# Kernel tuning notes

Hardware: AMD Instinct MI355X
Metric: run time of the kernel (lower is better)

The kernel has to match this reference:

```python
import jax, jax.numpy as jnp
import numpy as np


def setup_inputs() -> dict:
    key = jax.random.key(0)
    k1, k2 = jax.random.split(key)
    N, K, D = 400000, 50, 256
    locF = jax.random.normal(k1, (N, 1, D), dtype=jnp.float32)
    Ck = jax.random.normal(k2, (1, K, D), dtype=jnp.float32)
    return {"locF": locF, "Ck": Ck}


def reference(locF, Ck):
    # locF: [N, 1, D], Ck: [1, k, D]
    x = locF[:, 0, :]            # [N, D]
    c = Ck[0]                    # [k, D]
    k, D = c.shape
    # mean squared distance: ((x - c)**2).mean(-1) expanded to avoid [N,k,D] intermediate
    x2 = jnp.sum(x * x, axis=1, keepdims=True)        # [N, 1]
    c2 = jnp.sum(c * c, axis=1)                       # [k]
    d2 = (x2 - 2.0 * (x @ c.T) + c2) / D              # [N, k]
    index = jnp.argmin(d2, axis=1)                    # [N]
    # single-pass scatter-add of sums and counts keyed by argmin
    sums = jax.ops.segment_sum(x, index, num_segments=k)   # [k, D]
    counts = jnp.zeros((k,), dtype=jnp.int32).at[index].add(1)
    Ck1 = sums[None]            # [1, k, D]  (matches torch.cat along dim=1 of [1,1,D] chunks)
    nItems = counts[None]       # [1, k]
    return Ck1, nItems
```

## Files before the change

kernel.cpp:

```cpp
#include <hip/hip_runtime.h>


typedef _Float16 f16x8 __attribute__((ext_vector_type(8)));
typedef float    f32x4 __attribute__((ext_vector_type(4)));
typedef float    f32x16 __attribute__((ext_vector_type(16)));
typedef int      i32x4 __attribute__((ext_vector_type(4)));
typedef unsigned int u32x4 __attribute__((ext_vector_type(4)));

constexpr int K = 50, KP = 64, D = 256, KD = K * D;
constexpr int BLK = 1024, GRID = 512, CH = 32;
constexpr int SST = 68;

#define VMCNT0 asm volatile("s_waitcnt vmcnt(0)" ::: "memory")
#define LGKM0  asm volatile("s_waitcnt lgkmcnt(0)" ::: "memory")
#define SBAR   { __builtin_amdgcn_sched_barrier(0); __builtin_amdgcn_s_barrier(); __builtin_amdgcn_sched_barrier(0); }

__global__ __launch_bounds__(BLK)
void k_fused(const float* __restrict__ x, const float* __restrict__ cc,
             float* __restrict__ partial, float* __restrict__ out,
             int N, int useAtomic) {
    __shared__ _Float16       sC[K * D];
    __shared__ unsigned short sxh[2][CH * D];
    __shared__ float          sS0[32 * SST];
    __shared__ float          sS1[32 * SST];
    __shared__ float          sc2[KP];
    __shared__ int            sidx[2][CH];
    __shared__ int            scnt[K];

    const int tid = threadIdx.x;
    for (int i = tid; i < K * D; i += BLK) sC[i] = (_Float16)0.f;
    if (tid < K) scnt[tid] = 0;
    __syncthreads();
    for (int i = tid; i < KD; i += BLK) {
        int r = i >> 8, col = i & 255, ch = col >> 3, wd = col & 7;
        sC[r * D + (((ch ^ (r & 7)) << 3) | wd)] = (_Float16)cc[i];
    }
    if (tid < KP) {
        float s = 0.f;
        if (tid < K) for (int q = 0; q < D; ++q) { float v = cc[tid * D + q]; s += v * v; }
        sc2[tid] = s;
    }
    __syncthreads();

    const int lane = tid & 63, ci = lane & 15, g = lane >> 4, w = tid >> 6;
    const int kh   = (w >= 14) ? 1 : 0;
    const int wA   = w & 1;
    const int ra   = lane & 31;
    const int dl   = lane >> 5;
    const int rakey = (ra & 7) ^ (((ra >> 3) & 1) << 2);
    const int cl32 = wA * 32 + (lane & 31);
    const int clkey = (lane & 31) & 7;
    const _Float16* cbp = &sC[(cl32 < K ? cl32 : K - 1) * D];
    const int bcol = w * 16 + ci, bc3 = bcol >> 3, bce = bcol & 7;

    const int nCh = N / CH;
    const int cpb = nCh / gridDim.x, rem = nCh % gridDim.x;
    const int bid = blockIdx.x;
    const int lo  = bid * cpb + (bid < rem ? bid : rem);
    const int cnt = cpb + (bid < rem ? 1 : 0);

    const float INF = 3.4e38f;
    const float c2A = (cl32 < K) ? sc2[cl32] : INF;

    const int srow = 2 * w + (lane >> 5);
    const int scol = (lane & 31);
    const int skey = (srow & 7) ^ (((srow >> 3) & 1) << 2);
    f32x4 rA = {0,0,0,0}, rB = {0,0,0,0};
#define ISSUE(t_) { const float* b_ = x + (size_t)(t_) * (CH * D) + srow * D + 8 * scol; \
    rA = *(const f32x4*)(b_); rB = *(const f32x4*)(b_ + 4); }
#define WSLOT(s_) { \
    f16x8 h_ = {(_Float16)rA[0], (_Float16)rA[1], (_Float16)rA[2], (_Float16)rA[3], \
                (_Float16)rB[0], (_Float16)rB[1], (_Float16)rB[2], (_Float16)rB[3]}; \
    *(f16x8*)(&sxh[s_][srow * D + ((scol ^ skey) << 3)]) = h_; }

    f32x4 bacc0 = {0,0,0,0}, bacc1 = {0,0,0,0}, bacc2 = {0,0,0,0}, bacc3 = {0,0,0,0};

    if (cnt > 0) { ISSUE(lo) VMCNT0; WSLOT(0) if (cnt > 1) ISSUE(lo + 1) }
    LGKM0; SBAR;

    for (int i = 0; i <= cnt; ++i) {
        if (w >= 12 && i < cnt) {
            const unsigned short* xb = &sxh[i & 1][0];
            f32x16 acc = {0,0,0,0,0,0,0,0,0,0,0,0,0,0,0,0};
#define A_KS(s) { \
            const int c_ = (kh * 8 + (s)) * 2 + dl; \
            f16x8 a = *(const f16x8*)(&xb[ra * D + ((c_ ^ rakey) << 3)]); \
            f16x8 b = *(const f16x8*)(cbp + ((c_ ^ clkey) << 3)); \
            acc = __builtin_amdgcn_mfma_f32_32x32x16_f16(a, b, acc, 0, 0, 0); }
            A_KS(0) A_KS(1) A_KS(2) A_KS(3) A_KS(4) A_KS(5) A_KS(6) A_KS(7)
#undef A_KS
            if (kh == 0) {
#define DUMP(r) { const int row_ = ((r) & 3) + 8 * ((r) >> 2) + 4 * dl; \
                sS0[row_ * SST + cl32] = c2A - 2.f * acc[r]; }
                DUMP(0) DUMP(1) DUMP(2) DUMP(3) DUMP(4) DUMP(5) DUMP(6) DUMP(7)
                DUMP(8) DUMP(9) DUMP(10) DUMP(11) DUMP(12) DUMP(13) DUMP(14) DUMP(15)
#undef DUMP
            } else {
#define DUMP(r) { const int row_ = ((r) & 3) + 8 * ((r) >> 2) + 4 * dl; \
                sS1[row_ * SST + cl32] = -2.f * acc[r]; }
                DUMP(0) DUMP(1) DUMP(2) DUMP(3) DUMP(4) DUMP(5) DUMP(6) DUMP(7)
                DUMP(8) DUMP(9) DUMP(10) DUMP(11) DUMP(12) DUMP(13) DUMP(14) DUMP(15)
#undef DUMP
            }
        }

        if (i >= 1) {
            const unsigned short* xbh = &sxh[(i - 1) & 1][0];
            const int jb = (i - 1) & 1;
            i32x4 idA = *(const i32x4*)(&sidx[jb][8 * g]);
            i32x4 idB = *(const i32x4*)(&sidx[jb][8 * g + 4]);
            unsigned short v0, v1, v2, v3, v4, v5, v6, v7;
#define RDH(j) { const int p_ = 8 * g + (j); const int key_ = (j) ^ ((g & 1) << 2); \
            v##j = xbh[p_ * D + ((bc3 ^ key_) << 3) + bce]; }
            RDH(0) RDH(1) RDH(2) RDH(3) RDH(4) RDH(5) RDH(6) RDH(7)
#undef RDH
            unsigned int w0 = (unsigned int)v0 | ((unsigned int)v1 << 16);
            unsigned int w1 = (unsigned int)v2 | ((unsigned int)v3 << 16);
            unsigned int w2 = (unsigned int)v4 | ((unsigned int)v5 << 16);
            unsigned int w3 = (unsigned int)v6 | ((unsigned int)v7 << 16);
            u32x4 W = {w0, w1, w2, w3};
            f16x8 bfr = __builtin_bit_cast(f16x8, W);
#define BMT(M, ACC) { \
            const int cl_ = (M) * 16 + ci; \
            f16x8 a = {(_Float16)(idA[0] == cl_ ? 1.f : 0.f), (_Float16)(idA[1] == cl_ ? 1.f : 0.f), \
                       (_Float16)(idA[2] == cl_ ? 1.f : 0.f), (_Float16)(idA[3] == cl_ ? 1.f : 0.f), \
                       (_Float16)(idB[0] == cl_ ? 1.f : 0.f), (_Float16)(idB[1] == cl_ ? 1.f : 0.f), \
                       (_Float16)(idB[2] == cl_ ? 1.f : 0.f), (_Float16)(idB[3] == cl_ ? 1.f : 0.f)}; \
            ACC = __builtin_amdgcn_mfma_f32_16x16x32_f16(a, bfr, ACC, 0, 0, 0); }
            BMT(0, bacc0) BMT(1, bacc1) BMT(2, bacc2) BMT(3, bacc3)
#undef BMT
        }

        LGKM0; SBAR;

        if (i + 1 < cnt) {
            VMCNT0;
            WSLOT((i + 1) & 1)
            if (i + 2 < cnt) ISSUE(lo + i + 2)
        }

        if (w >= 8 && w < 12 && i < cnt) {
            const int p_ = (w - 8) * 8 + (lane >> 3);
            const int q  = lane & 7;
            const float* s0p = &sS0[p_ * SST + 8 * q];
            const float* s1p = &sS1[p_ * SST + 8 * q];
            f32x4 a0 = *(const f32x4*)(s0p), a1 = *(const f32x4*)(s0p + 4);
            f32x4 b0 = *(const f32x4*)(s1p), b1 = *(const f32x4*)(s1p + 4);
            f32x4 u = a0 + b0, v = a1 + b1;
            float bm = u[0]; int bb = 8 * q;
#define CMP(VV, E, OFF) { float s_ = VV[E]; int c_ = 8 * q + (OFF); \
            if (s_ < bm) { bm = s_; bb = c_; } }
            CMP(u,1,1) CMP(u,2,2) CMP(u,3,3)
            CMP(v,0,4) CMP(v,1,5) CMP(v,2,6) CMP(v,3,7)
#undef CMP
            { float pm = __shfl_xor(bm, 1, 64); int pb = __shfl_xor(bb, 1, 64);
              if (pm < bm || (pm == bm && pb < bb)) { bm = pm; bb = pb; } }
            { float pm = __shfl_xor(bm, 2, 64); int pb = __shfl_xor(bb, 2, 64);
              if (pm < bm || (pm == bm && pb < bb)) { bm = pm; bb = pb; } }
            { float pm = __shfl_xor(bm, 4, 64); int pb = __shfl_xor(bb, 4, 64);
              if (pm < bm || (pm == bm && pb < bb)) { bm = pm; bb = pb; } }
            if (q == 0) { sidx[i & 1][p_] = bb; atomicAdd(&scnt[bb], 1); }
        }
        LGKM0; SBAR;
    }

    if (useAtomic) {
#define WBK(M, ACC) { \
        { int cl_ = (M)*16 + 4*g + 0; if (cl_ < K) atomicAdd(&out[cl_ * D + bcol], ACC[0]); } \
        { int cl_ = (M)*16 + 4*g + 1; if (cl_ < K) atomicAdd(&out[cl_ * D + bcol], ACC[1]); } \
        { int cl_ = (M)*16 + 4*g + 2; if (cl_ < K) atomicAdd(&out[cl_ * D + bcol], ACC[2]); } \
        { int cl_ = (M)*16 + 4*g + 3; if (cl_ < K) atomicAdd(&out[cl_ * D + bcol], ACC[3]); } }
        WBK(0, bacc0) WBK(1, bacc1) WBK(2, bacc2) WBK(3, bacc3)
#undef WBK
    } else {
        float* pb = partial + (size_t)bid * KD;
#define WBK(M, ACC) { \
        { int cl_ = (M)*16 + 4*g + 0; if (cl_ < K) pb[cl_ * D + bcol] = ACC[0]; } \
        { int cl_ = (M)*16 + 4*g + 1; if (cl_ < K) pb[cl_ * D + bcol] = ACC[1]; } \
        { int cl_ = (M)*16 + 4*g + 2; if (cl_ < K) pb[cl_ * D + bcol] = ACC[2]; } \
        { int cl_ = (M)*16 + 4*g + 3; if (cl_ < K) pb[cl_ * D + bcol] = ACC[3]; } }
        WBK(0, bacc0) WBK(1, bacc1) WBK(2, bacc2) WBK(3, bacc3)
#undef WBK
    }
    __syncthreads();
    for (int k = tid; k < K; k += BLK) atomicAdd(&out[KD + k], (float)scnt[k]);
}

__global__ __launch_bounds__(256)
void k_reduce(const float* __restrict__ partial, float* __restrict__ out, int G) {
    const int j  = blockIdx.x * 256 + threadIdx.x;
    const int bs = G / 8;
    const int b0 = blockIdx.y * bs;
    float s = 0.f;
    for (int b = b0; b < b0 + bs; ++b) s += partial[(size_t)b * KD + j];
    atomicAdd(&out[j], s);
}

extern "C" void kernel_launch(void* const* d_in, const int* in_sizes, int n_in,
                              void* d_out, int out_size, void* d_ws, size_t ws_size,
                              hipStream_t stream) {
    const float* x = (const float*)d_in[0];
    const float* c = (const float*)d_in[1];
    float* out = (float*)d_out;
    const int N = in_sizes[0] / D;

    float* partial = (float*)d_ws;
    const size_t need = (size_t)GRID * KD * sizeof(float);
    const int useAtomic = (ws_size < need) ? 1 : 0;

    hipMemsetAsync(d_out, 0, (size_t)out_size * sizeof(float), stream);
    k_fused<<<GRID, BLK, 0, stream>>>(x, c, partial, out, N, useAtomic);
    if (!useAtomic) {
        k_reduce<<<dim3(KD / 256, 8), 256, 0, stream>>>(partial, out, GRID);
    }
}
```

Baseline: 136.7 us.

## Materialize one-hot assignment matrix in LDS and store distance scores in fp16

The argmin stage now writes a 1 into a double-buffered fp16 one-hot matrix in LDS instead of storing cluster indices. The scatter-MFMA therefore loads its A fragment directly rather than building it with per-lane compares, and spare waves zero the next buffer each iteration. Partial distance scores are also stored in LDS as fp16 rather than fp32, which halves LDS traffic for the argmin reads. The scatter-MFMA block is moved ahead of the distance MFMA in the loop. Storing scores in fp16 lowers precision and may flip near-tie argmin decisions.

```diff
diff --git a/kernel.cpp b/kernel.cpp
--- a/kernel.cpp
+++ b/kernel.cpp
@@ -4,12 +4,12 @@
 typedef _Float16 f16x8 __attribute__((ext_vector_type(8)));
 typedef float    f32x4 __attribute__((ext_vector_type(4)));
 typedef float    f32x16 __attribute__((ext_vector_type(16)));
-typedef int      i32x4 __attribute__((ext_vector_type(4)));
 typedef unsigned int u32x4 __attribute__((ext_vector_type(4)));
 
 constexpr int K = 50, KP = 64, D = 256, KD = K * D;
 constexpr int BLK = 1024, GRID = 512, CH = 32;
-constexpr int SST = 68;
+constexpr int SSTH = 72;
+constexpr int PST  = 40;
 
 #define VMCNT0 asm volatile("s_waitcnt vmcnt(0)" ::: "memory")
 #define LGKM0  asm volatile("s_waitcnt lgkmcnt(0)" ::: "memory")
@@ -21,14 +21,15 @@
              int N, int useAtomic) {
     __shared__ _Float16       sC[K * D];
     __shared__ unsigned short sxh[2][CH * D];
-    __shared__ float          sS0[32 * SST];
-    __shared__ float          sS1[32 * SST];
+    __shared__ alignas(16) _Float16 sS0[32 * SSTH];
+    __shared__ alignas(16) _Float16 sS1[32 * SSTH];
+    __shared__ alignas(16) _Float16 sPT[2][64 * PST];
     __shared__ float          sc2[KP];
-    __shared__ int            sidx[2][CH];
     __shared__ int            scnt[K];
 
     const int tid = threadIdx.x;
     for (int i = tid; i < K * D; i += BLK) sC[i] = (_Float16)0.f;
+    for (int i = tid; i < 2 * 64 * PST; i += BLK) sPT[0][i] = (_Float16)0.f;
     if (tid < K) scnt[tid] = 0;
     __syncthreads();
     for (int i = tid; i < KD; i += BLK) {
@@ -79,6 +80,27 @@
     LGKM0; SBAR;
 
     for (int i = 0; i <= cnt; ++i) {
+        if (i >= 1) {
+            const unsigned short* xbh = &sxh[(i - 1) & 1][0];
+            const _Float16* pt = &sPT[(i - 1) & 1][0];
+            unsigned short v0, v1, v2, v3, v4, v5, v6, v7;
+#define RDH(j) { const int p_ = 8 * g + (j); const int key_ = (j) ^ ((g & 1) << 2); \
+            v##j = xbh[p_ * D + ((bc3 ^ key_) << 3) + bce]; }
+            RDH(0) RDH(1) RDH(2) RDH(3) RDH(4) RDH(5) RDH(6) RDH(7)
+#undef RDH
+            unsigned int w0 = (unsigned int)v0 | ((unsigned int)v1 << 16);
+            unsigned int w1 = (unsigned int)v2 | ((unsigned int)v3 << 16);
+            unsigned int w2 = (unsigned int)v4 | ((unsigned int)v5 << 16);
+            unsigned int w3 = (unsigned int)v6 | ((unsigned int)v7 << 16);
+            u32x4 W = {w0, w1, w2, w3};
+            f16x8 bfr = __builtin_bit_cast(f16x8, W);
+#define BMT(M, ACC) { \
+            f16x8 a = *(const f16x8*)(pt + ((M) * 16 + ci) * PST + 8 * g); \
+            ACC = __builtin_amdgcn_mfma_f32_16x16x32_f16(a, bfr, ACC, 0, 0, 0); }
+            BMT(0, bacc0) BMT(1, bacc1) BMT(2, bacc2) BMT(3, bacc3)
+#undef BMT
+        }
+
         if (w >= 12 && i < cnt) {
             const unsigned short* xb = &sxh[i & 1][0];
             f32x16 acc = {0,0,0,0,0,0,0,0,0,0,0,0,0,0,0,0};
@@ -91,46 +113,19 @@
 #undef A_KS
             if (kh == 0) {
 #define DUMP(r) { const int row_ = ((r) & 3) + 8 * ((r) >> 2) + 4 * dl; \
-                sS0[row_ * SST + cl32] = c2A - 2.f * acc[r]; }
+                sS0[row_ * SSTH + cl32] = (_Float16)(c2A - 2.f * acc[r]); }
                 DUMP(0) DUMP(1) DUMP(2) DUMP(3) DUMP(4) DUMP(5) DUMP(6) DUMP(7)
                 DUMP(8) DUMP(9) DUMP(10) DUMP(11) DUMP(12) DUMP(13) DUMP(14) DUMP(15)
 #undef DUMP
             } else {
 #define DUMP(r) { const int row_ = ((r) & 3) + 8 * ((r) >> 2) + 4 * dl; \
-                sS1[row_ * SST + cl32] = -2.f * acc[r]; }
+                sS1[row_ * SSTH + cl32] = (_Float16)(-2.f * acc[r]); }
                 DUMP(0) DUMP(1) DUMP(2) DUMP(3) DUMP(4) DUMP(5) DUMP(6) DUMP(7)
                 DUMP(8) DUMP(9) DUMP(10) DUMP(11) DUMP(12) DUMP(13) DUMP(14) DUMP(15)
 #undef DUMP
             }
         }
 
-        if (i >= 1) {
-            const unsigned short* xbh = &sxh[(i - 1) & 1][0];
-            const int jb = (i - 1) & 1;
-            i32x4 idA = *(const i32x4*)(&sidx[jb][8 * g]);
-            i32x4 idB = *(const i32x4*)(&sidx[jb][8 * g + 4]);
-            unsigned short v0, v1, v2, v3, v4, v5, v6, v7;
-#define RDH(j) { const int p_ = 8 * g + (j); const int key_ = (j) ^ ((g & 1) << 2); \
-            v##j = xbh[p_ * D + ((bc3 ^ key_) << 3) + bce]; }
-            RDH(0) RDH(1) RDH(2) RDH(3) RDH(4) RDH(5) RDH(6) RDH(7)
-#undef RDH
-            unsigned int w0 = (unsigned int)v0 | ((unsigned int)v1 << 16);
-            unsigned int w1 = (unsigned int)v2 | ((unsigned int)v3 << 16);
-            unsigned int w2 = (unsigned int)v4 | ((unsigned int)v5 << 16);
-            unsigned int w3 = (unsigned int)v6 | ((unsigned int)v7 << 16);
-            u32x4 W = {w0, w1, w2, w3};
-            f16x8 bfr = __builtin_bit_cast(f16x8, W);
-#define BMT(M, ACC) { \
-            const int cl_ = (M) * 16 + ci; \
-            f16x8 a = {(_Float16)(idA[0] == cl_ ? 1.f : 0.f), (_Float16)(idA[1] == cl_ ? 1.f : 0.f), \
-                       (_Float16)(idA[2] == cl_ ? 1.f : 0.f), (_Float16)(idA[3] == cl_ ? 1.f : 0.f), \
-                       (_Float16)(idB[0] == cl_ ? 1.f : 0.f), (_Float16)(idB[1] == cl_ ? 1.f : 0.f), \
-                       (_Float16)(idB[2] == cl_ ? 1.f : 0.f), (_Float16)(idB[3] == cl_ ? 1.f : 0.f)}; \
-            ACC = __builtin_amdgcn_mfma_f32_16x16x32_f16(a, bfr, ACC, 0, 0, 0); }
-            BMT(0, bacc0) BMT(1, bacc1) BMT(2, bacc2) BMT(3, bacc3)
-#undef BMT
-        }
-
         LGKM0; SBAR;
 
         if (i + 1 < cnt) {
@@ -139,19 +134,26 @@
             if (i + 2 < cnt) ISSUE(lo + i + 2)
         }
 
+        if (w < 8 && i + 1 < cnt) {
+            const int z = w * 64 + lane;
+            if (z < (64 * PST * 2) / 16) {
+                f16x8 zz = {(_Float16)0.f,(_Float16)0.f,(_Float16)0.f,(_Float16)0.f,
+                            (_Float16)0.f,(_Float16)0.f,(_Float16)0.f,(_Float16)0.f};
+                *(f16x8*)(&sPT[(i + 1) & 1][z * 8]) = zz;
+            }
+        }
+
         if (w >= 8 && w < 12 && i < cnt) {
             const int p_ = (w - 8) * 8 + (lane >> 3);
             const int q  = lane & 7;
-            const float* s0p = &sS0[p_ * SST + 8 * q];
-            const float* s1p = &sS1[p_ * SST + 8 * q];
-            f32x4 a0 = *(const f32x4*)(s0p), a1 = *(const f32x4*)(s0p + 4);
-            f32x4 b0 = *(const f32x4*)(s1p), b1 = *(const f32x4*)(s1p + 4);
-            f32x4 u = a0 + b0, v = a1 + b1;
-            float bm = u[0]; int bb = 8 * q;
-#define CMP(VV, E, OFF) { float s_ = VV[E]; int c_ = 8 * q + (OFF); \
+            const _Float16* s0p = &sS0[p_ * SSTH + 8 * q];
+            const _Float16* s1p = &sS1[p_ * SSTH + 8 * q];
+            f16x8 h0 = *(const f16x8*)(s0p);
+            f16x8 h1 = *(const f16x8*)(s1p);
+            float bm = (float)h0[0] + (float)h1[0]; int bb = 8 * q;
+#define CMP(E) { float s_ = (float)h0[E] + (float)h1[E]; int c_ = 8 * q + (E); \
             if (s_ < bm) { bm = s_; bb = c_; } }
-            CMP(u,1,1) CMP(u,2,2) CMP(u,3,3)
-            CMP(v,0,4) CMP(v,1,5) CMP(v,2,6) CMP(v,3,7)
+            CMP(1) CMP(2) CMP(3) CMP(4) CMP(5) CMP(6) CMP(7)
 #undef CMP
             { float pm = __shfl_xor(bm, 1, 64); int pb = __shfl_xor(bb, 1, 64);
               if (pm < bm || (pm == bm && pb < bb)) { bm = pm; bb = pb; } }
@@ -159,7 +161,10 @@
               if (pm < bm || (pm == bm && pb < bb)) { bm = pm; bb = pb; } }
             { float pm = __shfl_xor(bm, 4, 64); int pb = __shfl_xor(bb, 4, 64);
               if (pm < bm || (pm == bm && pb < bb)) { bm = pm; bb = pb; } }
-            if (q == 0) { sidx[i & 1][p_] = bb; atomicAdd(&scnt[bb], 1); }
+            if (q == 0) {
+                sPT[i & 1][bb * PST + p_] = (_Float16)1.f;
+                atomicAdd(&scnt[bb], 1);
+            }
         }
         LGKM0; SBAR;
     }
```

New measurement: 135.4 us. About the same (-1.0%).
